# Performance work log

Hardware: AMD Instinct MI355X
Metric: run time of the kernel (lower is better)

Reference implementation:

```python
import math
import jax, jax.numpy as jnp
import numpy as np

B, S, H, NH = 4, 2048, 1024, 16
HD = H // NH
SCALE = math.sqrt(H)  # module divides by sqrt(hidden_dim), not sqrt(head_dim)


def setup_inputs() -> dict:
    key = jax.random.key(0)
    ks = jax.random.split(key, 9)
    lim = 1.0 / math.sqrt(H)
    def lin(kw, kb):
        W = jax.random.uniform(kw, (H, H), jnp.float32, -lim, lim)
        b = jax.random.uniform(kb, (H,), jnp.float32, -lim, lim)
        return W, b
    Wq, bq = lin(ks[0], ks[1])
    Wk, bk = lin(ks[2], ks[3])
    Wv, bv = lin(ks[4], ks[5])
    Wo, bo = lin(ks[6], ks[7])
    hidden_states = jax.random.normal(ks[8], (B, S, H), jnp.float32)
    masks = jnp.ones((B, S), jnp.float32)
    return {"hidden_states": hidden_states, "masks": masks,
            "Wq": Wq, "bq": bq, "Wk": Wk, "bk": bk,
            "Wv": Wv, "bv": bv, "Wo": Wo, "bo": bo}


def reference(hidden_states, masks, Wq, bq, Wk, bk, Wv, bv, Wo, bo):
    bsz, msl, hdim = hidden_states.shape
    def proj(W, b):
        # [b, s, h] -> [b, nh, s, hd]
        y = hidden_states @ W.T + b
        return y.reshape(bsz, msl, NH, HD).transpose(0, 2, 1, 3)
    q = proj(Wq, bq)
    k = proj(Wk, bk)
    v = proj(Wv, bv)
    scores = jnp.einsum('bnqd,bnkd->bnqk', q, k) / SCALE
    # mask outer product: [b,1,q,k], zero where either token is padded
    m2 = (masks[:, None, :, None] * masks[:, None, None, :])
    scores = jnp.where(m2 == 0, jnp.float32(-1e12), scores)
    attn = jax.nn.softmax(scores, axis=-1)
    ctx = jnp.einsum('bnqk,bnkd->bnqd', attn, v)
    ctx = ctx.transpose(0, 2, 1, 3).reshape(bsz, msl, hdim)
    return ctx @ Wo.T + bo
```

## Files before the change

### kernel.cpp

```cpp
#include <hip/hip_runtime.h>
#include <hip/hip_bf16.h>
#include <stdint.h>

typedef unsigned short u16;
typedef __attribute__((ext_vector_type(4))) float f32x4;
typedef __attribute__((ext_vector_type(8))) short bf16x8;
typedef __attribute__((ext_vector_type(4))) unsigned int u32x4;

#define GLL16(src, dst) __builtin_amdgcn_global_load_lds( \
    (const __attribute__((address_space(1))) void*)(src), \
    (__attribute__((address_space(3))) void*)(dst), 16, 0, 0)

static __device__ __forceinline__ u16 f2bf(float x) {
    uint32_t u = __builtin_bit_cast(uint32_t, x);
    u += 0x7fffu + ((u >> 16) & 1u);
    return (u16)(u >> 16);
}

static __device__ __forceinline__ uint32_t cvtpk(float lo, float hi) {
    uint32_t r;
    asm("v_cvt_pk_bf16_f32 %0, %1, %2" : "=v"(r) : "v"(lo), "v"(hi));
    return r;
}

__global__ __launch_bounds__(256) void cvt_f32_bf16(
        const float* __restrict__ in, u16* __restrict__ out, int n4) {
    int i = blockIdx.x * 256 + threadIdx.x;
    if (i >= n4) return;
    float4 v = ((const float4*)in)[i];
    ushort4 o;
    o.x = f2bf(v.x); o.y = f2bf(v.y); o.z = f2bf(v.z); o.w = f2bf(v.w);
    ((ushort4*)out)[i] = o;
}

__global__ __launch_bounds__(256) void cvt_w4(
        const float* __restrict__ s0, const float* __restrict__ s1,
        const float* __restrict__ s2, const float* __restrict__ s3,
        u16* __restrict__ dst) {
    int wsel = blockIdx.y;
    const float* s = (wsel == 0) ? s0 : (wsel == 1) ? s1 : (wsel == 2) ? s2 : s3;
    int i = blockIdx.x * 256 + threadIdx.x;
    float4 v = ((const float4*)s)[i];
    ushort4 o;
    o.x = f2bf(v.x); o.y = f2bf(v.y); o.z = f2bf(v.z); o.w = f2bf(v.w);
    ((ushort4*)(dst + (size_t)wsel * 1024 * 1024))[i] = o;
}

__global__ __launch_bounds__(256, 2) void gemm_qkv(
        const u16* __restrict__ A, const u16* __restrict__ W,
        const float* __restrict__ bq, const float* __restrict__ bk,
        const float* __restrict__ bv,
        u16* __restrict__ Qo, u16* __restrict__ Ko, u16* __restrict__ Vo) {
    __shared__ __align__(16) u16 As[2][128 * 32];
    __shared__ __align__(16) u16 Bs[2][128 * 32];
    const int tid = threadIdx.x;
    const int lane = tid & 63;
    const int w = tid >> 6, wm = w >> 1, wn = w & 1;
    const int l15 = lane & 15, l4 = lane >> 4;
    int v = (blockIdx.x & 7) * 192 + (blockIdx.x >> 3);
    int vy = v / 24, vx = v - vy * 24;
    const int m0 = vy * 128, n0 = vx * 128;
    const float SC2 = 0.03125f * 1.44269504088896f;

    f32x4 acc[4][4];
#pragma unroll
    for (int i = 0; i < 4; i++)
#pragma unroll
        for (int j = 0; j < 4; j++) acc[i][j] = f32x4{0.f, 0.f, 0.f, 0.f};

#define QKV_STAGE(buf, kt) do {                                            \
    _Pragma("unroll")                                                      \
    for (int i_ = 0; i_ < 2; i_++) {                                       \
        int c_ = tid + i_ * 256;                                           \
        int row_ = c_ >> 2, slot_ = c_ & 3;                                \
        int cc_ = slot_ ^ ((row_ >> 1) & 3);                               \
        GLL16(A + (size_t)(m0 + row_) * 1024 + (kt) + cc_ * 8, As[buf] + c_ * 8); \
    }                                                                      \
    _Pragma("unroll")                                                      \
    for (int i_ = 0; i_ < 2; i_++) {                                       \
        int c_ = tid + i_ * 256;                                           \
        int row_ = c_ >> 2, slot_ = c_ & 3;                                \
        int cc_ = slot_ ^ ((row_ >> 1) & 3);                               \
        GLL16(W + (size_t)(n0 + row_) * 1024 + (kt) + cc_ * 8, Bs[buf] + c_ * 8); \
    }                                                                      \
} while (0)

    QKV_STAGE(0, 0);
    __syncthreads();

    for (int kt = 0; kt < 1024; kt += 32) {
        const int cur = (kt >> 5) & 1;
        if (kt != 992) QKV_STAGE(cur ^ 1, kt + 32);

        bf16x8 af[4], bfr[4];
#pragma unroll
        for (int i = 0; i < 4; i++) {
            int row = wm * 64 + i * 16 + l15;
            int slot = l4 ^ ((row >> 1) & 3);
            af[i] = *(const bf16x8*)(As[cur] + row * 32 + slot * 8);
        }
#pragma unroll
        for (int j = 0; j < 4; j++) {
            int row = wn * 64 + j * 16 + l15;
            int slot = l4 ^ ((row >> 1) & 3);
            bfr[j] = *(const bf16x8*)(Bs[cur] + row * 32 + slot * 8);
        }
#pragma unroll
        for (int i = 0; i < 4; i++)
#pragma unroll
            for (int j = 0; j < 4; j++)
                acc[i][j] = __builtin_amdgcn_mfma_f32_16x16x32_bf16(af[i], bfr[j], acc[i][j], 0, 0, 0);
        __syncthreads();
    }
#undef QKV_STAGE

#pragma unroll
    for (int j = 0; j < 4; j++) {
        int col = n0 + wn * 64 + j * 16 + l15;
        int sel = col >> 10;
        float bvv = (sel == 0) ? bq[col] : (sel == 1) ? bk[col - 1024] : bv[col - 2048];
#pragma unroll
        for (int i = 0; i < 4; i++) {
            int rowb = m0 + wm * 64 + i * 16 + l4 * 4;
            if (sel == 0) {
#pragma unroll
                for (int r = 0; r < 4; r++)
                    Qo[(size_t)(rowb + r) * 1024 + col] = f2bf((acc[i][j][r] + bvv) * SC2);
            } else if (sel == 1) {
#pragma unroll
                for (int r = 0; r < 4; r++)
                    Ko[(size_t)(rowb + r) * 1024 + (col - 1024)] = f2bf(acc[i][j][r] + bvv);
            } else {
                int cc = col - 2048;
                int bb = rowb >> 11;
                int sp = ((m0 + wm * 64) & 2047) + (i >> 1) * 32 + l4 * 8 + (i & 1) * 4;
                int hh = cc >> 6, dd = cc & 63;
                ushort4 o;
                o.x = f2bf(acc[i][j][0] + bvv);
                o.y = f2bf(acc[i][j][1] + bvv);
                o.z = f2bf(acc[i][j][2] + bvv);
                o.w = f2bf(acc[i][j][3] + bvv);
                *(ushort4*)(Vo + ((size_t)((bb * 16 + hh) * 64 + dd)) * 2048 + sp) = o;
            }
        }
    }
}

__global__ __launch_bounds__(256, 2) void gemm_o(
        const u16* __restrict__ A, const u16* __restrict__ W,
        const float* __restrict__ bias, float* __restrict__ out) {
    __shared__ __align__(16) u16 As[2][128 * 32];
    __shared__ __align__(16) u16 Bs[2][128 * 32];
    const int tid = threadIdx.x;
    const int lane = tid & 63;
    const int w = tid >> 6, wm = w >> 1, wn = w & 1;
    const int l15 = lane & 15, l4 = lane >> 4;
    int v = (blockIdx.x & 7) * 64 + (blockIdx.x >> 3);
    int vy = v >> 3, vx = v & 7;
    const int m0 = vy * 128, n0 = vx * 128;

    f32x4 acc[4][4];
#pragma unroll
    for (int i = 0; i < 4; i++)
#pragma unroll
        for (int j = 0; j < 4; j++) acc[i][j] = f32x4{0.f, 0.f, 0.f, 0.f};

#define O_STAGE(buf, kt) do {                                              \
    _Pragma("unroll")                                                      \
    for (int i_ = 0; i_ < 2; i_++) {                                       \
        int c_ = tid + i_ * 256;                                           \
        int row_ = c_ >> 2, slot_ = c_ & 3;                                \
        int cc_ = slot_ ^ ((row_ >> 1) & 3);                               \
        GLL16(A + (size_t)(m0 + row_) * 1024 + (kt) + cc_ * 8, As[buf] + c_ * 8); \
    }                                                                      \
    _Pragma("unroll")                                                      \
    for (int i_ = 0; i_ < 2; i_++) {                                       \
        int c_ = tid + i_ * 256;                                           \
        int row_ = c_ >> 2, slot_ = c_ & 3;                                \
        int cc_ = slot_ ^ ((row_ >> 1) & 3);                               \
        GLL16(W + (size_t)(n0 + row_) * 1024 + (kt) + cc_ * 8, Bs[buf] + c_ * 8); \
    }                                                                      \
} while (0)

    O_STAGE(0, 0);
    __syncthreads();

    for (int kt = 0; kt < 1024; kt += 32) {
        const int cur = (kt >> 5) & 1;
        if (kt != 992) O_STAGE(cur ^ 1, kt + 32);

        bf16x8 af[4], bfr[4];
#pragma unroll
        for (int i = 0; i < 4; i++) {
            int row = wm * 64 + i * 16 + l15;
            int slot = l4 ^ ((row >> 1) & 3);
            af[i] = *(const bf16x8*)(As[cur] + row * 32 + slot * 8);
        }
#pragma unroll
        for (int j = 0; j < 4; j++) {
            int row = wn * 64 + j * 16 + l15;
            int slot = l4 ^ ((row >> 1) & 3);
            bfr[j] = *(const bf16x8*)(Bs[cur] + row * 32 + slot * 8);
        }
#pragma unroll
        for (int i = 0; i < 4; i++)
#pragma unroll
            for (int j = 0; j < 4; j++)
                acc[i][j] = __builtin_amdgcn_mfma_f32_16x16x32_bf16(af[i], bfr[j], acc[i][j], 0, 0, 0);
        __syncthreads();
    }
#undef O_STAGE

#pragma unroll
    for (int j = 0; j < 4; j++) {
        int col = n0 + wn * 64 + j * 16 + l15;
        float bvv = bias[col];
#pragma unroll
        for (int i = 0; i < 4; i++) {
            int rowb = m0 + wm * 64 + i * 16 + l4 * 4;
#pragma unroll
            for (int r = 0; r < 4; r++)
                out[(size_t)(rowb + r) * 1024 + col] = acc[i][j][r] + bvv;
        }
    }
}

__global__ __launch_bounds__(256, 3) void attn_fused(
        const u16* __restrict__ Q, const u16* __restrict__ K,
        const u16* __restrict__ Vt, const float* __restrict__ mask,
        u16* __restrict__ ctx) {
    __shared__ __align__(16) u16 Ks[2][64 * 64];
    __shared__ __align__(16) u16 Vs[2][64 * 64];

    const int tid = threadIdx.x, lane = tid & 63, w = tid >> 6;
    const int l15 = lane & 15, l4 = lane >> 4;
    const int bid = blockIdx.x;
    const int inner = bid >> 3;
    const int bh = ((inner >> 4) << 3) | (bid & 7);
    const int b = bh >> 4, h = bh & 15;
    const int qw = (inner & 15) * 128 + w * 32;
    const float THR2 = 8.0f;

    const u16* Qg = Q + (size_t)b * 2048 * 1024 + h * 64;
    const u16* Kg = K + (size_t)b * 2048 * 1024 + h * 64;
    const u16* Vg = Vt + (size_t)bh * 64 * 2048;
    const float* mp = mask + b * 2048;

    bool anym;
    {
        bool bad = false;
#pragma unroll
        for (int i = 0; i < 8; i++) {
            float4 a = ((const float4*)mp)[lane * 8 + i];
            bad |= (a.x == 0.f) | (a.y == 0.f) | (a.z == 0.f) | (a.w == 0.f);
        }
        anym = (__ballot(bad) != 0ull);
    }

#define STAGE_KV(buf, kvbase) do {                                         \
    _Pragma("unroll")                                                      \
    for (int i_ = 0; i_ < 2; i_++) {                                       \
        int c_ = tid + i_ * 256;                                           \
        int row_ = c_ >> 3, slot_ = c_ & 7;                                \
        int cc_ = slot_ ^ (row_ & 7);                                      \
        GLL16(Kg + (size_t)((kvbase) + row_) * 1024 + cc_ * 8, Ks[buf] + c_ * 8); \
    }                                                                      \
    _Pragma("unroll")                                                      \
    for (int i_ = 0; i_ < 2; i_++) {                                       \
        int c_ = tid + i_ * 256;                                           \
        int row_ = c_ >> 3, slot_ = c_ & 7;                                \
        int cc_ = slot_ ^ (row_ & 7);                                      \
        GLL16(Vg + (size_t)row_ * 2048 + (kvbase) + cc_ * 8, Vs[buf] + c_ * 8); \
    }                                                                      \
} while (0)

    bf16x8 qfr[2][2];
#pragma unroll
    for (int qi = 0; qi < 2; qi++)
#pragma unroll
        for (int kf = 0; kf < 2; kf++)
            qfr[qi][kf] = *(const bf16x8*)(Qg + (size_t)(qw + qi * 16 + l15) * 1024 + kf * 32 + l4 * 8);

    float mq01[2];
#pragma unroll
    for (int qi = 0; qi < 2; qi++)
        mq01[qi] = (mp[qw + qi * 16 + l15] != 0.f) ? 1.f : 0.f;

    float m_run[2] = {0.f, 0.f};
    f32x4 acc_l[2];
    f32x4 oaccT[4][2];
#pragma unroll
    for (int qi = 0; qi < 2; qi++) acc_l[qi] = f32x4{0.f, 0.f, 0.f, 0.f};
#pragma unroll
    for (int df = 0; df < 4; df++)
#pragma unroll
        for (int qi = 0; qi < 2; qi++) oaccT[df][qi] = f32x4{0.f, 0.f, 0.f, 0.f};

    const u32x4 ones4 = u32x4{0x3F803F80u, 0x3F803F80u, 0x3F803F80u, 0x3F803F80u};
    const bf16x8 ones = __builtin_bit_cast(bf16x8, ones4);

    STAGE_KV(0, 0);
    __syncthreads();

    for (int it = 0; it < 32; ++it) {
        const int cur = it & 1;
        const int kv0 = it * 64;

        if (it != 31) STAGE_KV(cur ^ 1, kv0 + 64);

        bf16x8 kfr[4][2];
#pragma unroll
        for (int kvf = 0; kvf < 4; kvf++)
#pragma unroll
            for (int kf = 0; kf < 2; kf++) {
                int row = kvf * 16 + l15;
                int slot = (kf * 4 + l4) ^ (row & 7);
                kfr[kvf][kf] = *(const bf16x8*)(Ks[cur] + row * 64 + slot * 8);
            }
        f32x4 p[4][2];
#pragma unroll
        for (int kvf = 0; kvf < 4; kvf++)
#pragma unroll
            for (int qi = 0; qi < 2; qi++) p[kvf][qi] = f32x4{0.f, 0.f, 0.f, 0.f};
        __builtin_amdgcn_s_setprio(1);
#pragma unroll
        for (int kvf = 0; kvf < 4; kvf++)
#pragma unroll
            for (int qi = 0; qi < 2; qi++)
#pragma unroll
                for (int kf = 0; kf < 2; kf++)
                    p[kvf][qi] = __builtin_amdgcn_mfma_f32_16x16x32_bf16(kfr[kvf][kf], qfr[qi][kf], p[kvf][qi], 0, 0, 0);
        __builtin_amdgcn_s_setprio(0);

        if (anym) {
            float4 mkv[4];
#pragma unroll
            for (int kvf = 0; kvf < 4; kvf++)
                mkv[kvf] = ((const float4*)(mp + kv0))[kvf * 4 + l4];
#pragma unroll
            for (int qi = 0; qi < 2; qi++)
#pragma unroll
                for (int kvf = 0; kvf < 4; kvf++)
#pragma unroll
                    for (int r = 0; r < 4; r++) {
                        float bb = (mkv[kvf][r] != 0.f) ? 0.f : -1e12f;
                        p[kvf][qi][r] = __builtin_fmaf(p[kvf][qi][r], mq01[qi], bb);
                    }
        }

        float t[2];
#pragma unroll
        for (int qi = 0; qi < 2; qi++) {
            float a0 = fmaxf(fmaxf(p[0][qi][0], p[0][qi][1]), fmaxf(p[0][qi][2], p[0][qi][3]));
            float a1 = fmaxf(fmaxf(p[1][qi][0], p[1][qi][1]), fmaxf(p[1][qi][2], p[1][qi][3]));
            float a2 = fmaxf(fmaxf(p[2][qi][0], p[2][qi][1]), fmaxf(p[2][qi][2], p[2][qi][3]));
            float a3 = fmaxf(fmaxf(p[3][qi][0], p[3][qi][1]), fmaxf(p[3][qi][2], p[3][qi][3]));
            t[qi] = fmaxf(fmaxf(a0, a1), fmaxf(a2, a3));
        }
        if (!__all((t[0] <= m_run[0] + THR2) && (t[1] <= m_run[1] + THR2))) {
#pragma unroll
            for (int qi = 0; qi < 2; qi++) {
                float tt = fmaxf(t[qi], __shfl_xor(t[qi], 16));
                tt = fmaxf(tt, __shfl_xor(tt, 32));
                float mn = fmaxf(m_run[qi], tt);
                float sc = __builtin_amdgcn_exp2f(m_run[qi] - mn);
                m_run[qi] = mn;
                acc_l[qi] *= sc;
#pragma unroll
                for (int df = 0; df < 4; df++) oaccT[df][qi] *= sc;
            }
        }
        if (__all((m_run[0] == 0.f) & (m_run[1] == 0.f))) {
#pragma unroll
            for (int qi = 0; qi < 2; qi++)
#pragma unroll
                for (int kvf = 0; kvf < 4; kvf++)
#pragma unroll
                    for (int r = 0; r < 4; r++)
                        p[kvf][qi][r] = __builtin_amdgcn_exp2f(p[kvf][qi][r]);
        } else {
#pragma unroll
            for (int qi = 0; qi < 2; qi++)
#pragma unroll
                for (int kvf = 0; kvf < 4; kvf++)
#pragma unroll
                    for (int r = 0; r < 4; r++)
                        p[kvf][qi][r] = __builtin_amdgcn_exp2f(p[kvf][qi][r] - m_run[qi]);
        }

        bf16x8 pb[2][2];
#pragma unroll
        for (int qi = 0; qi < 2; qi++)
#pragma unroll
            for (int kf = 0; kf < 2; kf++) {
                u32x4 tq;
                tq.x = cvtpk(p[2 * kf][qi][0], p[2 * kf][qi][1]);
                tq.y = cvtpk(p[2 * kf][qi][2], p[2 * kf][qi][3]);
                tq.z = cvtpk(p[2 * kf + 1][qi][0], p[2 * kf + 1][qi][1]);
                tq.w = cvtpk(p[2 * kf + 1][qi][2], p[2 * kf + 1][qi][3]);
                pb[qi][kf] = __builtin_bit_cast(bf16x8, tq);
            }

        bf16x8 vfr[4][2];
#pragma unroll
        for (int df = 0; df < 4; df++)
#pragma unroll
            for (int kf = 0; kf < 2; kf++) {
                int row = df * 16 + l15;
                int slot = (kf * 4 + l4) ^ (row & 7);
                vfr[df][kf] = *(const bf16x8*)(Vs[cur] + row * 64 + slot * 8);
            }

        __builtin_amdgcn_s_setprio(1);
#pragma unroll
        for (int df = 0; df < 4; df++)
#pragma unroll
            for (int qi = 0; qi < 2; qi++)
#pragma unroll
                for (int kf = 0; kf < 2; kf++)
                    oaccT[df][qi] = __builtin_amdgcn_mfma_f32_16x16x32_bf16(vfr[df][kf], pb[qi][kf], oaccT[df][qi], 0, 0, 0);
#pragma unroll
        for (int qi = 0; qi < 2; qi++)
#pragma unroll
            for (int kf = 0; kf < 2; kf++)
                acc_l[qi] = __builtin_amdgcn_mfma_f32_16x16x32_bf16(ones, pb[qi][kf], acc_l[qi], 0, 0, 0);
        __builtin_amdgcn_s_setprio(0);

        __syncthreads();
    }

#pragma unroll
    for (int qi = 0; qi < 2; qi++) {
        float rl = 1.0f / acc_l[qi][0];
        int tok = qw + qi * 16 + l15;
#pragma unroll
        for (int df = 0; df < 4; df++) {
            uint2 o;
            o.x = cvtpk(oaccT[df][qi][0] * rl, oaccT[df][qi][1] * rl);
            o.y = cvtpk(oaccT[df][qi][2] * rl, oaccT[df][qi][3] * rl);
            *(uint2*)(ctx + (size_t)(b * 2048 + tok) * 1024 + h * 64 + df * 16 + l4 * 4) = o;
        }
    }
#undef STAGE_KV
}

extern "C" void kernel_launch(void* const* d_in, const int* in_sizes, int n_in,
                              void* d_out, int out_size, void* d_ws, size_t ws_size,
                              hipStream_t stream) {
    const float* hs    = (const float*)d_in[0];
    const float* masks = (const float*)d_in[1];
    const float* Wq = (const float*)d_in[2];
    const float* bq = (const float*)d_in[3];
    const float* Wk = (const float*)d_in[4];
    const float* bk = (const float*)d_in[5];
    const float* Wv = (const float*)d_in[6];
    const float* bv = (const float*)d_in[7];
    const float* Wo = (const float*)d_in[8];
    const float* bo = (const float*)d_in[9];

    const int NT = 4 * 2048;
    const int H = 1024;

    u16* hs_b = (u16*)d_ws;
    u16* w_b  = hs_b + (size_t)NT * H;
    u16* wo_b = w_b + (size_t)3 * H * H;
    u16* Qb   = w_b + (size_t)4 * H * H;
    u16* Kb   = Qb + (size_t)NT * H;
    u16* Vtb  = Kb + (size_t)NT * H;
    u16* Cb   = hs_b;

    cvt_f32_bf16<<<NT * H / 1024, 256, 0, stream>>>(hs, hs_b, NT * H / 4);
    cvt_w4<<<dim3(H * H / 1024, 4), 256, 0, stream>>>(Wq, Wk, Wv, Wo, w_b);

    gemm_qkv<<<1536, 256, 0, stream>>>(hs_b, w_b, bq, bk, bv, Qb, Kb, Vtb);

    attn_fused<<<1024, 256, 0, stream>>>(Qb, Kb, Vtb, masks, Cb);

    gemm_o<<<512, 256, 0, stream>>>(Cb, wo_b, bo, (float*)d_out);
}
```

Before: 197.1 us.

## Process two query sub-tiles per attention block to reuse staged K/V tiles

Each attention block now covers 256 query rows instead of 128. Every wave handles two 32-row query groups and reuses the same K/V fragments loaded from shared memory for both. This halves the grid and the global K/V staging traffic per query row, and it shares the V fragment reads. In exchange the kernel needs roughly twice the accumulator registers, so launch bounds drop to 2 blocks per SM, with lower occupancy and fewer blocks for load balancing.

```diff
diff --git a/kernel.cpp b/kernel.cpp
--- a/kernel.cpp
+++ b/kernel.cpp
@@ -175,7 +175,7 @@
     }                                                                      \
     _Pragma("unroll")                                                      \
     for (int i_ = 0; i_ < 2; i_++) {                                       \
-        int c_ = tid + i_ * 256;                                           \
+        int c_ = tid + i_ * 256;                                       \
         int row_ = c_ >> 2, slot_ = c_ & 3;                                \
         int cc_ = slot_ ^ ((row_ >> 1) & 3);                               \
         GLL16(W + (size_t)(n0 + row_) * 1024 + (kt) + cc_ * 8, Bs[buf] + c_ * 8); \
@@ -225,7 +225,7 @@
     }
 }
 
-__global__ __launch_bounds__(256, 3) void attn_fused(
+__global__ __launch_bounds__(256, 2) void attn_fused(
         const u16* __restrict__ Q, const u16* __restrict__ K,
         const u16* __restrict__ Vt, const float* __restrict__ mask,
         u16* __restrict__ ctx) {
@@ -236,9 +236,9 @@
     const int l15 = lane & 15, l4 = lane >> 4;
     const int bid = blockIdx.x;
     const int inner = bid >> 3;
-    const int bh = ((inner >> 4) << 3) | (bid & 7);
+    const int bh = ((inner >> 3) << 3) | (bid & 7);
     const int b = bh >> 4, h = bh & 15;
-    const int qw = (inner & 15) * 128 + w * 32;
+    const int qbase = (inner & 7) * 256 + w * 32;
     const float THR2 = 8.0f;
 
     const u16* Qg = Q + (size_t)b * 2048 * 1024 + h * 64;
@@ -274,27 +274,35 @@
     }                                                                      \
 } while (0)
 
-    bf16x8 qfr[2][2];
-#pragma unroll
-    for (int qi = 0; qi < 2; qi++)
-#pragma unroll
-        for (int kf = 0; kf < 2; kf++)
-            qfr[qi][kf] = *(const bf16x8*)(Qg + (size_t)(qw + qi * 16 + l15) * 1024 + kf * 32 + l4 * 8);
-
-    float mq01[2];
-#pragma unroll
-    for (int qi = 0; qi < 2; qi++)
-        mq01[qi] = (mp[qw + qi * 16 + l15] != 0.f) ? 1.f : 0.f;
-
-    float m_run[2] = {0.f, 0.f};
-    f32x4 acc_l[2];
-    f32x4 oaccT[4][2];
-#pragma unroll
-    for (int qi = 0; qi < 2; qi++) acc_l[qi] = f32x4{0.f, 0.f, 0.f, 0.f};
-#pragma unroll
-    for (int df = 0; df < 4; df++)
-#pragma unroll
-        for (int qi = 0; qi < 2; qi++) oaccT[df][qi] = f32x4{0.f, 0.f, 0.f, 0.f};
+    bf16x8 qfr[2][2][2];
+#pragma unroll
+    for (int qh = 0; qh < 2; qh++)
+#pragma unroll
+        for (int qi = 0; qi < 2; qi++)
+#pragma unroll
+            for (int kf = 0; kf < 2; kf++)
+                qfr[qh][qi][kf] = *(const bf16x8*)(Qg +
+                    (size_t)(qbase + qh * 128 + qi * 16 + l15) * 1024 + kf * 32 + l4 * 8);
+
+    float mq01[2][2];
+#pragma unroll
+    for (int qh = 0; qh < 2; qh++)
+#pragma unroll
+        for (int qi = 0; qi < 2; qi++)
+            mq01[qh][qi] = (mp[qbase + qh * 128 + qi * 16 + l15] != 0.f) ? 1.f : 0.f;
+
+    float m_run[2][2] = {{0.f, 0.f}, {0.f, 0.f}};
+    f32x4 acc_l[2][2];
+    f32x4 oaccT[2][4][2];
+#pragma unroll
+    for (int qh = 0; qh < 2; qh++) {
+#pragma unroll
+        for (int qi = 0; qi < 2; qi++) acc_l[qh][qi] = f32x4{0.f, 0.f, 0.f, 0.f};
+#pragma unroll
+        for (int df = 0; df < 4; df++)
+#pragma unroll
+            for (int qi = 0; qi < 2; qi++) oaccT[qh][df][qi] = f32x4{0.f, 0.f, 0.f, 0.f};
+    }
 
     const u32x4 ones4 = u32x4{0x3F803F80u, 0x3F803F80u, 0x3F803F80u, 0x3F803F80u};
     const bf16x8 ones = __builtin_bit_cast(bf16x8, ones4);
@@ -317,130 +325,141 @@
                 int slot = (kf * 4 + l4) ^ (row & 7);
                 kfr[kvf][kf] = *(const bf16x8*)(Ks[cur] + row * 64 + slot * 8);
             }
-        f32x4 p[4][2];
-#pragma unroll
-        for (int kvf = 0; kvf < 4; kvf++)
-#pragma unroll
-            for (int qi = 0; qi < 2; qi++) p[kvf][qi] = f32x4{0.f, 0.f, 0.f, 0.f};
-        __builtin_amdgcn_s_setprio(1);
-#pragma unroll
-        for (int kvf = 0; kvf < 4; kvf++)
+        bf16x8 vfr[4][2];
+
+#pragma unroll
+        for (int qh = 0; qh < 2; qh++) {
+            f32x4 p[4][2];
+#pragma unroll
+            for (int kvf = 0; kvf < 4; kvf++)
+#pragma unroll
+                for (int qi = 0; qi < 2; qi++) p[kvf][qi] = f32x4{0.f, 0.f, 0.f, 0.f};
+            __builtin_amdgcn_s_setprio(1);
+#pragma unroll
+            for (int kvf = 0; kvf < 4; kvf++)
+#pragma unroll
+                for (int qi = 0; qi < 2; qi++)
+#pragma unroll
+                    for (int kf = 0; kf < 2; kf++)
+                        p[kvf][qi] = __builtin_amdgcn_mfma_f32_16x16x32_bf16(
+                            kfr[kvf][kf], qfr[qh][qi][kf], p[kvf][qi], 0, 0, 0);
+            __builtin_amdgcn_s_setprio(0);
+
+            if (qh == 0) {
+#pragma unroll
+                for (int df = 0; df < 4; df++)
+#pragma unroll
+                    for (int kf = 0; kf < 2; kf++) {
+                        int row = df * 16 + l15;
+                        int slot = (kf * 4 + l4) ^ (row & 7);
+                        vfr[df][kf] = *(const bf16x8*)(Vs[cur] + row * 64 + slot * 8);
+                    }
+            }
+
+            if (anym) {
+                float4 mkv[4];
+#pragma unroll
+                for (int kvf = 0; kvf < 4; kvf++)
+                    mkv[kvf] = ((const float4*)(mp + kv0))[kvf * 4 + l4];
+#pragma unroll
+                for (int qi = 0; qi < 2; qi++)
+#pragma unroll
+                    for (int kvf = 0; kvf < 4; kvf++)
+#pragma unroll
+                        for (int r = 0; r < 4; r++) {
+                            float bb = (mkv[kvf][r] != 0.f) ? 0.f : -1e12f;
+                            p[kvf][qi][r] = __builtin_fmaf(p[kvf][qi][r], mq01[qh][qi], bb);
+                        }
+            }
+
+            float t[2];
+#pragma unroll
+            for (int qi = 0; qi < 2; qi++) {
+                float a0 = fmaxf(fmaxf(p[0][qi][0], p[0][qi][1]), fmaxf(p[0][qi][2], p[0][qi][3]));
+                float a1 = fmaxf(fmaxf(p[1][qi][0], p[1][qi][1]), fmaxf(p[1][qi][2], p[1][qi][3]));
+                float a2 = fmaxf(fmaxf(p[2][qi][0], p[2][qi][1]), fmaxf(p[2][qi][2], p[2][qi][3]));
+                float a3 = fmaxf(fmaxf(p[3][qi][0], p[3][qi][1]), fmaxf(p[3][qi][2], p[3][qi][3]));
+                t[qi] = fmaxf(fmaxf(a0, a1), fmaxf(a2, a3));
+            }
+            if (!__all((t[0] <= m_run[qh][0] + THR2) && (t[1] <= m_run[qh][1] + THR2))) {
+#pragma unroll
+                for (int qi = 0; qi < 2; qi++) {
+                    float tt = fmaxf(t[qi], __shfl_xor(t[qi], 16));
+                    tt = fmaxf(tt, __shfl_xor(tt, 32));
+                    float mn = fmaxf(m_run[qh][qi], tt);
+                    float sc = __builtin_amdgcn_exp2f(m_run[qh][qi] - mn);
+                    m_run[qh][qi] = mn;
+                    acc_l[qh][qi] *= sc;
+#pragma unroll
+                    for (int df = 0; df < 4; df++) oaccT[qh][df][qi] *= sc;
+                }
+            }
+            if (__all((m_run[qh][0] == 0.f) & (m_run[qh][1] == 0.f))) {
+#pragma unroll
+                for (int qi = 0; qi < 2; qi++)
+#pragma unroll
+                    for (int kvf = 0; kvf < 4; kvf++)
+#pragma unroll
+                        for (int r = 0; r < 4; r++)
+                            p[kvf][qi][r] = __builtin_amdgcn_exp2f(p[kvf][qi][r]);
+            } else {
+#pragma unroll
+                for (int qi = 0; qi < 2; qi++)
+#pragma unroll
+                    for (int kvf = 0; kvf < 4; kvf++)
+#pragma unroll
+                        for (int r = 0; r < 4; r++)
+                            p[kvf][qi][r] = __builtin_amdgcn_exp2f(p[kvf][qi][r] - m_run[qh][qi]);
+            }
+
+            bf16x8 pb[2][2];
 #pragma unroll
             for (int qi = 0; qi < 2; qi++)
 #pragma unroll
+                for (int kf = 0; kf < 2; kf++) {
+                    u32x4 tq;
+                    tq.x = cvtpk(p[2 * kf][qi][0], p[2 * kf][qi][1]);
+                    tq.y = cvtpk(p[2 * kf][qi][2], p[2 * kf][qi][3]);
+                    tq.z = cvtpk(p[2 * kf + 1][qi][0], p[2 * kf + 1][qi][1]);
+                    tq.w = cvtpk(p[2 * kf + 1][qi][2], p[2 * kf + 1][qi][3]);
+                    pb[qi][kf] = __builtin_bit_cast(bf16x8, tq);
+                }
+
+            __builtin_amdgcn_s_setprio(1);
+#pragma unroll
+            for (int df = 0; df < 4; df++)
+#pragma unroll
+                for (int qi = 0; qi < 2; qi++)
+#pragma unroll
+                    for (int kf = 0; kf < 2; kf++)
+                        oaccT[qh][df][qi] = __builtin_amdgcn_mfma_f32_16x16x32_bf16(
+                            vfr[df][kf], pb[qi][kf], oaccT[qh][df][qi], 0, 0, 0);
+#pragma unroll
+            for (int qi = 0; qi < 2; qi++)
+#pragma unroll
                 for (int kf = 0; kf < 2; kf++)
-                    p[kvf][qi] = __builtin_amdgcn_mfma_f32_16x16x32_bf16(kfr[kvf][kf], qfr[qi][kf], p[kvf][qi], 0, 0, 0);
-        __builtin_amdgcn_s_setprio(0);
-
-        if (anym) {
-            float4 mkv[4];
-#pragma unroll
-            for (int kvf = 0; kvf < 4; kvf++)
-                mkv[kvf] = ((const float4*)(mp + kv0))[kvf * 4 + l4];
-#pragma unroll
-            for (int qi = 0; qi < 2; qi++)
-#pragma unroll
-                for (int kvf = 0; kvf < 4; kvf++)
-#pragma unroll
-                    for (int r = 0; r < 4; r++) {
-                        float bb = (mkv[kvf][r] != 0.f) ? 0.f : -1e12f;
-                        p[kvf][qi][r] = __builtin_fmaf(p[kvf][qi][r], mq01[qi], bb);
-                    }
-        }
-
-        float t[2];
+                    acc_l[qh][qi] = __builtin_amdgcn_mfma_f32_16x16x32_bf16(
+                        ones, pb[qi][kf], acc_l[qh][qi], 0, 0, 0);
+            __builtin_amdgcn_s_setprio(0);
+        }
+
+        __syncthreads();
+    }
+
+#pragma unroll
+    for (int qh = 0; qh < 2; qh++)
 #pragma unroll
         for (int qi = 0; qi < 2; qi++) {
-            float a0 = fmaxf(fmaxf(p[0][qi][0], p[0][qi][1]), fmaxf(p[0][qi][2], p[0][qi][3]));
-            float a1 = fmaxf(fmaxf(p[1][qi][0], p[1][qi][1]), fmaxf(p[1][qi][2], p[1][qi][3]));
-            float a2 = fmaxf(fmaxf(p[2][qi][0], p[2][qi][1]), fmaxf(p[2][qi][2], p[2][qi][3]));
-            float a3 = fmaxf(fmaxf(p[3][qi][0], p[3][qi][1]), fmaxf(p[3][qi][2], p[3][qi][3]));
-            t[qi] = fmaxf(fmaxf(a0, a1), fmaxf(a2, a3));
-        }
-        if (!__all((t[0] <= m_run[0] + THR2) && (t[1] <= m_run[1] + THR2))) {
-#pragma unroll
-            for (int qi = 0; qi < 2; qi++) {
-                float tt = fmaxf(t[qi], __shfl_xor(t[qi], 16));
-                tt = fmaxf(tt, __shfl_xor(tt, 32));
-                float mn = fmaxf(m_run[qi], tt);
-                float sc = __builtin_amdgcn_exp2f(m_run[qi] - mn);
-                m_run[qi] = mn;
-                acc_l[qi] *= sc;
-#pragma unroll
-                for (int df = 0; df < 4; df++) oaccT[df][qi] *= sc;
-            }
-        }
-        if (__all((m_run[0] == 0.f) & (m_run[1] == 0.f))) {
-#pragma unroll
-            for (int qi = 0; qi < 2; qi++)
-#pragma unroll
-                for (int kvf = 0; kvf < 4; kvf++)
-#pragma unroll
-                    for (int r = 0; r < 4; r++)
-                        p[kvf][qi][r] = __builtin_amdgcn_exp2f(p[kvf][qi][r]);
-        } else {
-#pragma unroll
-            for (int qi = 0; qi < 2; qi++)
-#pragma unroll
-                for (int kvf = 0; kvf < 4; kvf++)
-#pragma unroll
-                    for (int r = 0; r < 4; r++)
-                        p[kvf][qi][r] = __builtin_amdgcn_exp2f(p[kvf][qi][r] - m_run[qi]);
-        }
-
-        bf16x8 pb[2][2];
-#pragma unroll
-        for (int qi = 0; qi < 2; qi++)
-#pragma unroll
-            for (int kf = 0; kf < 2; kf++) {
-                u32x4 tq;
-                tq.x = cvtpk(p[2 * kf][qi][0], p[2 * kf][qi][1]);
-                tq.y = cvtpk(p[2 * kf][qi][2], p[2 * kf][qi][3]);
-                tq.z = cvtpk(p[2 * kf + 1][qi][0], p[2 * kf + 1][qi][1]);
-                tq.w = cvtpk(p[2 * kf + 1][qi][2], p[2 * kf + 1][qi][3]);
-                pb[qi][kf] = __builtin_bit_cast(bf16x8, tq);
-            }
-
-        bf16x8 vfr[4][2];
-#pragma unroll
-        for (int df = 0; df < 4; df++)
-#pragma unroll
-            for (int kf = 0; kf < 2; kf++) {
-                int row = df * 16 + l15;
-                int slot = (kf * 4 + l4) ^ (row & 7);
-                vfr[df][kf] = *(const bf16x8*)(Vs[cur] + row * 64 + slot * 8);
-            }
-
-        __builtin_amdgcn_s_setprio(1);
-#pragma unroll
-        for (int df = 0; df < 4; df++)
-#pragma unroll
-            for (int qi = 0; qi < 2; qi++)
-#pragma unroll
-                for (int kf = 0; kf < 2; kf++)
-                    oaccT[df][qi] = __builtin_amdgcn_mfma_f32_16x16x32_bf16(vfr[df][kf], pb[qi][kf], oaccT[df][qi], 0, 0, 0);
-#pragma unroll
-        for (int qi = 0; qi < 2; qi++)
-#pragma unroll
-            for (int kf = 0; kf < 2; kf++)
-                acc_l[qi] = __builtin_amdgcn_mfma_f32_16x16x32_bf16(ones, pb[qi][kf], acc_l[qi], 0, 0, 0);
-        __builtin_amdgcn_s_setprio(0);
-
-        __syncthreads();
-    }
-
-#pragma unroll
-    for (int qi = 0; qi < 2; qi++) {
-        float rl = 1.0f / acc_l[qi][0];
-        int tok = qw + qi * 16 + l15;
-#pragma unroll
-        for (int df = 0; df < 4; df++) {
-            uint2 o;
-            o.x = cvtpk(oaccT[df][qi][0] * rl, oaccT[df][qi][1] * rl);
-            o.y = cvtpk(oaccT[df][qi][2] * rl, oaccT[df][qi][3] * rl);
-            *(uint2*)(ctx + (size_t)(b * 2048 + tok) * 1024 + h * 64 + df * 16 + l4 * 4) = o;
-        }
-    }
+            float rl = 1.0f / acc_l[qh][qi][0];
+            int tok = qbase + qh * 128 + qi * 16 + l15;
+#pragma unroll
+            for (int df = 0; df < 4; df++) {
+                uint2 o;
+                o.x = cvtpk(oaccT[qh][df][qi][0] * rl, oaccT[qh][df][qi][1] * rl);
+                o.y = cvtpk(oaccT[qh][df][qi][2] * rl, oaccT[qh][df][qi][3] * rl);
+                *(uint2*)(ctx + (size_t)(b * 2048 + tok) * 1024 + h * 64 + df * 16 + l4 * 4) = o;
+            }
+        }
 #undef STAGE_KV
 }
 
@@ -474,7 +493,7 @@
 
     gemm_qkv<<<1536, 256, 0, stream>>>(hs_b, w_b, bq, bk, bv, Qb, Kb, Vtb);
 
-    attn_fused<<<1024, 256, 0, stream>>>(Qb, Kb, Vtb, masks, Cb);
+    attn_fused<<<512, 256, 0, stream>>>(Qb, Kb, Vtb, masks, Cb);
 
     gemm_o<<<512, 256, 0, stream>>>(Cb, wo_b, bo, (float*)d_out);
 }
```

Result: no change. 199.4 us (+1.2%).
